# Optimization experiments

Hardware: AMD Instinct MI355X
Metric: run time of the kernel (lower is better)

The kernel has to match this reference:

```python
import jax, jax.numpy as jnp
import numpy as np

D = 1024
H = 16
HD = D // H
EPS = 1e-5

def _layernorm(x, g, b):
    mu = jnp.mean(x, axis=-1, keepdims=True)
    var = jnp.mean(jnp.square(x - mu), axis=-1, keepdims=True)
    return (x - mu) * jax.lax.rsqrt(var + EPS) * g + b

def setup_inputs() -> dict:
    key = jax.random.key(0)
    ks = jax.random.split(key, 12)
    B, Sq, Skv = 8, 1024, 1024
    s = 1.0 / np.sqrt(D)  # xavier-ish scale
    return {
        "Q": jax.random.normal(ks[0], (B, Sq, D), jnp.float32),
        "K": jax.random.normal(ks[1], (B, Skv, D), jnp.float32),
        "key_padding_mask": jnp.ones((B, Skv), jnp.int32),
        "Wq": jax.random.normal(ks[2], (D, D), jnp.float32) * s,
        "bq": jnp.zeros((D,), jnp.float32),
        "Wk": jax.random.normal(ks[3], (D, D), jnp.float32) * s,
        "bk": jnp.zeros((D,), jnp.float32),
        "Wv": jax.random.normal(ks[4], (D, D), jnp.float32) * s,
        "bv": jnp.zeros((D,), jnp.float32),
        "Wp": jax.random.normal(ks[5], (D, D), jnp.float32) * s,
        "bp": jnp.zeros((D,), jnp.float32),
        "g0": jnp.ones((D,), jnp.float32),
        "beta0": jnp.zeros((D,), jnp.float32),
        "g1": jnp.ones((D,), jnp.float32),
        "beta1": jnp.zeros((D,), jnp.float32),
    }

def reference(Q, K, key_padding_mask, Wq, bq, Wk, bk, Wv, bv, Wp, bp, g0, beta0, g1, beta1):
    B, Sq, _ = Q.shape
    q = Q @ Wq + bq                      # [B,Sq,D]
    k = K @ Wk + bk                      # [B,Skv,D]
    v = K @ Wv + bv
    qh = q.reshape(B, Sq, H, HD).transpose(0, 2, 1, 3)   # [B,H,Sq,hd]
    kh = k.reshape(B, -1, H, HD).transpose(0, 2, 1, 3)   # [B,H,Skv,hd]
    vh = v.reshape(B, -1, H, HD).transpose(0, 2, 1, 3)
    attn = jnp.einsum('bhqd,bhkd->bhqk', qh, kh) / np.sqrt(HD)
    pad = (key_padding_mask == 0)[:, None, None, :]      # [B,1,1,Skv]
    attn = jnp.where(pad, -jnp.inf, attn)
    attn = jax.nn.softmax(attn, axis=-1)
    ctx = jnp.einsum('bhqk,bhkd->bhqd', attn, vh)        # [B,H,Sq,hd]
    ctx = ctx.transpose(0, 2, 1, 3).reshape(B, Sq, H * HD)
    o = _layernorm(q + ctx, g0, beta0)
    o = _layernorm(o + jax.nn.gelu(o @ Wp + bp, approximate=False), g1, beta1)
    return o
```

## Files before the change

kernel.cpp:

```cpp
#include <hip/hip_runtime.h>
#include <hip/hip_bf16.h>
#include <math.h>

#define DEV __device__ __forceinline__

typedef __bf16 bf16;
typedef __bf16 bf16x8 __attribute__((ext_vector_type(8)));
typedef __bf16 bf16x4 __attribute__((ext_vector_type(4)));
typedef __bf16 bf16x2 __attribute__((ext_vector_type(2)));
typedef float f32x4 __attribute__((ext_vector_type(4)));
typedef float f32x16 __attribute__((ext_vector_type(16)));
typedef int i32x2 __attribute__((ext_vector_type(2)));
typedef unsigned int u32;
typedef unsigned long long u64;

static constexpr int BATCH = 8, S = 1024, D = 1024, H = 16, HD = 64;
static constexpr int M = BATCH * S;

static constexpr float QSCALE = 0.18033688f;

DEV f32x4 mfma16(bf16x8 a, bf16x8 b, f32x4 c) {
  return __builtin_amdgcn_mfma_f32_16x16x32_bf16(a, b, c, 0, 0, 0);
}
DEV f32x16 mfma32(bf16x8 a, bf16x8 b, f32x16 c) {
  return __builtin_amdgcn_mfma_f32_32x32x16_bf16(a, b, c, 0, 0, 0);
}

DEV void gload_lds16(const void* g, void* l) {
  __builtin_amdgcn_global_load_lds(
      (__attribute__((address_space(1))) void*)(g),
      (__attribute__((address_space(3))) void*)(l), 16, 0, 0);
}

DEV bf16x8 lds_read8(const void* base, int byteoff) {
  return *(const bf16x8*)((const char*)base + byteoff);
}

DEV u32 packbf(float a, float b) {
  bf16x2 t = { (bf16)a, (bf16)b };
  return __builtin_bit_cast(u32, t);
}


__global__ void cvt_bf16_kernel(const float* __restrict__ in0, bf16* __restrict__ out0,
                                const float* __restrict__ in1, bf16* __restrict__ out1, int n) {
  const float* in = blockIdx.y ? in1 : in0;
  bf16* out = blockIdx.y ? out1 : out0;
  int i = (blockIdx.x * blockDim.x + threadIdx.x) * 4;
  int stride = gridDim.x * blockDim.x * 4;
  for (; i < n; i += stride) {
    float4 v = *(const float4*)(in + i);
    bf16x4 o = { (bf16)v.x, (bf16)v.y, (bf16)v.z, (bf16)v.w };
    *(bf16x4*)(out + i) = o;
  }
}

__global__ void transpose_cvt_kernel(const float* __restrict__ w0, bf16* __restrict__ o0,
                                     const float* __restrict__ w1, bf16* __restrict__ o1,
                                     const float* __restrict__ w2, bf16* __restrict__ o2,
                                     const float* __restrict__ w3, bf16* __restrict__ o3) {
  const int z = blockIdx.z;
  const float* in = z == 0 ? w0 : z == 1 ? w1 : z == 2 ? w2 : w3;
  bf16* out = z == 0 ? o0 : z == 1 ? o1 : z == 2 ? o2 : o3;
  __shared__ float t[32][33];
  int n0 = blockIdx.x * 32, k0 = blockIdx.y * 32;
  int tx = threadIdx.x, ty = threadIdx.y;
  for (int i = 0; i < 32; i += 8)
    t[ty + i][tx] = in[(size_t)(k0 + ty + i) * D + n0 + tx];
  __syncthreads();
  for (int i = 0; i < 32; i += 8)
    out[(size_t)(n0 + ty + i) * D + k0 + tx] = (bf16)t[tx][ty + i];
}


template<int MODE>
DEV void gemm_body(const bf16* A, const bf16* Bt, const float* bias,
                   float* Cf, bf16* Cb, float osc,
                   bf16* As, bf16* Bs) {
  constexpr int K = 1024, N = 1024, BK = 32;
  const int tid = threadIdx.x, lane = tid & 63, wave = tid >> 6;
  int f = blockIdx.y * 8 + blockIdx.x;
  f = (f & 7) * 64 + (f >> 3);
  const int bm = f >> 3, bn = f & 7;
  const int wr = wave >> 1, wc = wave & 1;
  f32x4 acc[4][4] = {};
  const char* Ab = (const char*)(A + (size_t)bm * 128 * K);
  const char* Bb = (const char*)(Bt + (size_t)bn * 128 * K);

  for (int kt = 0; kt < K / BK; ++kt) {
    __syncthreads();
    const int k0b = kt * (BK * 2);
    for (int i = 0; i < 2; ++i) {
      int cbase = (wave * 2 + i) * 1024;
      int off = cbase + lane * 16;
      int row = off >> 6, col = off & 63;
      gload_lds16(Ab + (size_t)row * (K * 2) + k0b + col, (char*)As + cbase);
      gload_lds16(Bb + (size_t)row * (K * 2) + k0b + col, (char*)Bs + cbase);
    }
    __syncthreads();
    bf16x8 af[4], bfr[4];
    for (int mi = 0; mi < 4; ++mi)
      af[mi] = lds_read8(As, (wr * 64 + mi * 16 + (lane & 15)) * 64 + (lane >> 4) * 16);
    for (int ni = 0; ni < 4; ++ni)
      bfr[ni] = lds_read8(Bs, (wc * 64 + ni * 16 + (lane & 15)) * 64 + (lane >> 4) * 16);
    for (int mi = 0; mi < 4; ++mi)
      for (int ni = 0; ni < 4; ++ni)
        acc[mi][ni] = mfma16(af[mi], bfr[ni], acc[mi][ni]);
  }

  const int rbase = bm * 128 + wr * 64;
  const int cbase = bn * 128 + wc * 64;
  for (int ni = 0; ni < 4; ++ni) {
    int col = cbase + ni * 16 + (lane & 15);
    float bv = bias[col];
    for (int mi = 0; mi < 4; ++mi) {
      int row0 = rbase + mi * 16 + (lane >> 4) * 4;
      for (int r = 0; r < 4; ++r) {
        float v = acc[mi][ni][r] + bv;
        size_t idx = (size_t)(row0 + r) * N + col;
        if (MODE == 0) { Cf[idx] = v; Cb[idx] = (bf16)(v * osc); }
        if (MODE == 1) { Cb[idx] = (bf16)v; }
        if (MODE == 2) { Cf[idx] = v; }
      }
    }
  }
}

__global__ __launch_bounds__(256) void gemm_qkv_kernel(
    const bf16* __restrict__ Qb, const bf16* __restrict__ Kb,
    const bf16* __restrict__ Wqt, const bf16* __restrict__ Wkt, const bf16* __restrict__ Wvt,
    const float* __restrict__ bq, const float* __restrict__ bk, const float* __restrict__ bv,
    float* __restrict__ qf, bf16* __restrict__ qb,
    bf16* __restrict__ kb, bf16* __restrict__ vb)
{
  __shared__ bf16 As[128 * 32];
  __shared__ bf16 Bs[128 * 32];
  const int z = blockIdx.z;
  if (z == 0)      gemm_body<0>(Qb, Wqt, bq, qf, qb, QSCALE, As, Bs);
  else if (z == 1) gemm_body<1>(Kb, Wkt, bk, nullptr, kb, 1.f, As, Bs);
  else             gemm_body<1>(Kb, Wvt, bv, nullptr, vb, 1.f, As, Bs);
}

__global__ __launch_bounds__(256) void gemm_p_kernel(
    const bf16* __restrict__ A, const bf16* __restrict__ Bt,
    const float* __restrict__ bias, float* __restrict__ Cf)
{
  __shared__ bf16 As[128 * 32];
  __shared__ bf16 Bs[128 * 32];
  gemm_body<2>(A, Bt, bias, Cf, nullptr, 1.f, As, Bs);
}


DEV int swz(int row, int colb) { return row * 128 + (colb ^ ((row & 7) << 4)); }

__global__ __launch_bounds__(256, 3) void attn_kernel(
    const bf16* __restrict__ q, const bf16* __restrict__ k, const bf16* __restrict__ v,
    const int* __restrict__ mask, float* __restrict__ ctx)
{
  __shared__ bf16 Kl[2][64 * 64];
  __shared__ bf16 Vt[2][64 * 64];
  const int tid = threadIdx.x, lane = tid & 63, wave = tid >> 6;
  const int hi = lane >> 5, lq = lane & 31;
  const int wg = blockIdx.x;
  const int xcd = wg & 7, ix = wg >> 3;
  const int bh = xcd * 16 + (ix & 15);
  const int qt = ix >> 4;
  const int b = bh >> 4, h = bh & 15;
  const int q0 = qt * 128 + wave * 32;
  const size_t base = (size_t)b * S * D + (size_t)h * HD;

  bf16x8 qf[4];
#pragma unroll
  for (int hc = 0; hc < 4; ++hc)
    qf[hc] = *(const bf16x8*)(q + base + (size_t)(q0 + lq) * D + hc * 16 + hi * 8);

  f32x16 oaccT[2] = {};
  float mrow = -3e38f, lrow = 0.f;

  bf16x8 kst[2], vst[2];
  const int koff = tid * 16;
  const int krow = koff >> 7, kcol = koff & 127;

#define LOADK(KV0)                                                              \
  {                                                                             \
    _Pragma("unroll")                                                           \
    for (int rr = 0; rr < 2; ++rr)                                              \
      kst[rr] = *(const bf16x8*)((const char*)(k + base +                       \
                 (size_t)((KV0) + rr * 32 + krow) * D) + kcol);                 \
    _Pragma("unroll")                                                           \
    for (int rr = 0; rr < 2; ++rr) {                                            \
      int kvr = rr * 32 + wave * 8;                                             \
      _Pragma("unroll")                                                         \
      for (int i = 0; i < 8; ++i)                                               \
        vst[rr][i] = v[base + (size_t)((KV0) + kvr + i) * D + lane];            \
    }                                                                           \
  }

#define WRITEK(BI)                                                              \
  {                                                                             \
    _Pragma("unroll")                                                           \
    for (int rr = 0; rr < 2; ++rr)                                              \
      *(bf16x8*)((char*)Kl[BI] + swz(rr * 32 + krow, kcol)) = kst[rr];          \
    _Pragma("unroll")                                                           \
    for (int rr = 0; rr < 2; ++rr)                                              \
      *(bf16x8*)((char*)Vt[BI] + swz(lane, (rr * 32 + wave * 8) * 2)) = vst[rr];\
  }

  LOADK(0);
  WRITEK(0);

  for (int kt = 0; kt < S / 64; ++kt) {
    const int cur = kt & 1;
    const int kv0 = kt * 64;
    __syncthreads();
    if (kt < S / 64 - 1) LOADK(kv0 + 64);

    const char* Kb_ = (const char*)Kl[cur];
    const char* Vb_ = (const char*)Vt[cur];

    u64 mv = __ballot(mask[b * S + kv0 + lane] != 0);

    f32x16 sacc[2];
    __builtin_amdgcn_s_setprio(1);
#pragma unroll
    for (int sub = 0; sub < 2; ++sub) {
      f32x16 a = {};
#pragma unroll
      for (int hc = 0; hc < 4; ++hc) {
        bf16x8 kf = lds_read8(Kb_, swz(sub * 32 + lq, hc * 32 + hi * 16));
        a = mfma32(kf, qf[hc], a);
      }
      sacc[sub] = a;
    }
    __builtin_amdgcn_s_setprio(0);

    float mx = -3e38f;
    if (mv == ~0ull) {
#pragma unroll
      for (int sub = 0; sub < 2; ++sub)
#pragma unroll
        for (int r = 0; r < 16; ++r) mx = fmaxf(mx, sacc[sub][r]);
    } else {
      u64 mqh = mv >> (hi * 4);
#pragma unroll
      for (int sub = 0; sub < 2; ++sub)
#pragma unroll
        for (int rr = 0; rr < 4; ++rr)
#pragma unroll
          for (int rm = 0; rm < 4; ++rm) {
            int reg = rr * 4 + rm;
            bool ok = (mqh >> (rm + 8 * rr + 32 * sub)) & 1ull;
            float s = ok ? sacc[sub][reg] : -1e30f;
            sacc[sub][reg] = s;
            mx = fmaxf(mx, s);
          }
    }
    mx = fmaxf(mx, __shfl_xor(mx, 32));

    if (__any(mx > mrow + 11.5f)) {
      float mnew = fmaxf(mrow, mx);
      float fsc = exp2f(mrow - mnew);
      mrow = mnew;
      lrow *= fsc;
      oaccT[0] *= fsc;
      oaccT[1] *= fsc;
    }

    float rs = 0.f;
    u32 W[2][4][2];
#pragma unroll
    for (int sub = 0; sub < 2; ++sub)
#pragma unroll
      for (int rr = 0; rr < 4; ++rr)
#pragma unroll
        for (int hh = 0; hh < 2; ++hh) {
          float p0 = exp2f(sacc[sub][rr * 4 + 2 * hh] - mrow);
          float p1 = exp2f(sacc[sub][rr * 4 + 2 * hh + 1] - mrow);
          rs += p0 + p1;
          W[sub][rr][hh] = packbf(p0, p1);
        }
    rs += __shfl_xor(rs, 32);
    lrow += rs;

    bf16x8 pfr[4];
#pragma unroll
    for (int t = 0; t < 4; ++t) {
      const int sub = t >> 1, r0 = 2 * (t & 1);
      i32x2 s0 = __builtin_amdgcn_permlane32_swap(
          (int)W[sub][r0][0], (int)W[sub][r0 + 1][0], false, false);
      i32x2 s1 = __builtin_amdgcn_permlane32_swap(
          (int)W[sub][r0][1], (int)W[sub][r0 + 1][1], false, false);
      u32 wd[4] = { (u32)s0[0], (u32)s1[0], (u32)s0[1], (u32)s1[1] };
      pfr[t] = __builtin_bit_cast(bf16x8, wd);
    }

    __builtin_amdgcn_s_setprio(1);
#pragma unroll
    for (int hdsub = 0; hdsub < 2; ++hdsub) {
      f32x16 a = oaccT[hdsub];
#pragma unroll
      for (int t = 0; t < 4; ++t) {
        bf16x8 vf = lds_read8(Vb_, swz(hdsub * 32 + lq, t * 32 + hi * 16));
        a = mfma32(vf, pfr[t], a);
      }
      oaccT[hdsub] = a;
    }
    __builtin_amdgcn_s_setprio(0);

    if (kt < S / 64 - 1) WRITEK(cur ^ 1);
  }

  float linv = 1.0f / lrow;
  size_t rowb = ((size_t)b * S + q0 + lq) * D + (size_t)h * HD;
#pragma unroll
  for (int hdsub = 0; hdsub < 2; ++hdsub)
#pragma unroll
    for (int rr = 0; rr < 4; ++rr) {
      f32x4 o = { oaccT[hdsub][rr * 4 + 0] * linv, oaccT[hdsub][rr * 4 + 1] * linv,
                  oaccT[hdsub][rr * 4 + 2] * linv, oaccT[hdsub][rr * 4 + 3] * linv };
      *(f32x4*)(ctx + rowb + 32 * hdsub + 8 * rr + 4 * hi) = o;
    }
}


DEV void block_stats(float s, float s2, float* red, int tid, float& mu, float& rstd) {
  for (int off = 32; off > 0; off >>= 1) {
    s += __shfl_down(s, off);
    s2 += __shfl_down(s2, off);
  }
  int wave = tid >> 6, lane = tid & 63;
  if (lane == 0) { red[wave] = s; red[4 + wave] = s2; }
  __syncthreads();
  float S1 = red[0] + red[1] + red[2] + red[3];
  float S2 = red[4] + red[5] + red[6] + red[7];
  mu = S1 * (1.f / 1024.f);
  rstd = rsqrtf(S2 * (1.f / 1024.f) - mu * mu + 1e-5f);
}

__global__ __launch_bounds__(256) void ln0_kernel(
    const float* __restrict__ qf, const float* __restrict__ ctx,
    const float* __restrict__ g, const float* __restrict__ beta,
    float* __restrict__ of, bf16* __restrict__ ob)
{
  __shared__ float red[8];
  const int row = blockIdx.x, tid = threadIdx.x;
  const size_t base = (size_t)row * D;
  float4 x = *(const float4*)(qf + base + tid * 4);
  float4 c = *(const float4*)(ctx + base + tid * 4);
  x.x += c.x; x.y += c.y; x.z += c.z; x.w += c.w;
  float mu, rstd;
  block_stats(x.x + x.y + x.z + x.w,
              x.x * x.x + x.y * x.y + x.z * x.z + x.w * x.w, red, tid, mu, rstd);
  float4 gv = *(const float4*)(g + tid * 4);
  float4 bv = *(const float4*)(beta + tid * 4);
  float o0 = (x.x - mu) * rstd * gv.x + bv.x;
  float o1 = (x.y - mu) * rstd * gv.y + bv.y;
  float o2 = (x.z - mu) * rstd * gv.z + bv.z;
  float o3 = (x.w - mu) * rstd * gv.w + bv.w;
  *(float4*)(of + base + tid * 4) = make_float4(o0, o1, o2, o3);
  bf16x4 o = { (bf16)o0, (bf16)o1, (bf16)o2, (bf16)o3 };
  *(bf16x4*)(ob + base + tid * 4) = o;
}

DEV float gelu_exact(float t) { return 0.5f * t * (1.f + erff(t * 0.70710678118654752f)); }

__global__ __launch_bounds__(256) void ln1_kernel(
    const float* __restrict__ of, const float* __restrict__ pf,
    const float* __restrict__ g, const float* __restrict__ beta,
    float* __restrict__ out)
{
  __shared__ float red[8];
  const int row = blockIdx.x, tid = threadIdx.x;
  const size_t base = (size_t)row * D;
  float4 x = *(const float4*)(of + base + tid * 4);
  float4 p = *(const float4*)(pf + base + tid * 4);
  x.x += gelu_exact(p.x); x.y += gelu_exact(p.y);
  x.z += gelu_exact(p.z); x.w += gelu_exact(p.w);
  float mu, rstd;
  block_stats(x.x + x.y + x.z + x.w,
              x.x * x.x + x.y * x.y + x.z * x.z + x.w * x.w, red, tid, mu, rstd);
  float4 gv = *(const float4*)(g + tid * 4);
  float4 bv = *(const float4*)(beta + tid * 4);
  float o0 = (x.x - mu) * rstd * gv.x + bv.x;
  float o1 = (x.y - mu) * rstd * gv.y + bv.y;
  float o2 = (x.z - mu) * rstd * gv.z + bv.z;
  float o3 = (x.w - mu) * rstd * gv.w + bv.w;
  *(float4*)(out + base + tid * 4) = make_float4(o0, o1, o2, o3);
}


extern "C" void kernel_launch(void* const* d_in, const int* in_sizes, int n_in,
                              void* d_out, int out_size, void* d_ws, size_t ws_size,
                              hipStream_t stream) {
  const float* Q     = (const float*)d_in[0];
  const float* K     = (const float*)d_in[1];
  const int*   mask  = (const int*)d_in[2];
  const float* Wq    = (const float*)d_in[3];
  const float* bq    = (const float*)d_in[4];
  const float* Wk    = (const float*)d_in[5];
  const float* bk    = (const float*)d_in[6];
  const float* Wv    = (const float*)d_in[7];
  const float* bv    = (const float*)d_in[8];
  const float* Wp    = (const float*)d_in[9];
  const float* bp    = (const float*)d_in[10];
  const float* g0    = (const float*)d_in[11];
  const float* beta0 = (const float*)d_in[12];
  const float* g1    = (const float*)d_in[13];
  const float* beta1 = (const float*)d_in[14];
  float* out = (float*)d_out;

  char* w = (char*)d_ws;
  const size_t MB = 1u << 20;
  bf16* Qb  = (bf16*)(w + 0 * MB);
  bf16* Kb  = (bf16*)(w + 16 * MB);
  bf16* Wqt = (bf16*)(w + 32 * MB);
  bf16* Wkt = (bf16*)(w + 34 * MB);
  bf16* Wvt = (bf16*)(w + 36 * MB);
  bf16* Wpt = (bf16*)(w + 38 * MB);
  float* qf = (float*)(w + 40 * MB);
  bf16* qb  = (bf16*)(w + 72 * MB);
  bf16* kb  = (bf16*)(w + 88 * MB);
  bf16* vb  = (bf16*)(w + 104 * MB);
  float* ctx = (float*)(w + 120 * MB);
  float* pf  = ctx;
  float* of  = (float*)(w + 152 * MB);
  bf16* ob   = (bf16*)(w + 0 * MB);

  dim3 cg(1024, 2);
  cvt_bf16_kernel<<<cg, 256, 0, stream>>>(Q, Qb, K, Kb, M * D);
  dim3 tb(32, 8), tg(32, 32, 4);
  transpose_cvt_kernel<<<tg, tb, 0, stream>>>(Wq, Wqt, Wk, Wkt, Wv, Wvt, Wp, Wpt);

  dim3 gq(8, 64, 3);
  gemm_qkv_kernel<<<gq, 256, 0, stream>>>(Qb, Kb, Wqt, Wkt, Wvt, bq, bk, bv, qf, qb, kb, vb);

  attn_kernel<<<1024, 256, 0, stream>>>(qb, kb, vb, mask, ctx);

  ln0_kernel<<<M, 256, 0, stream>>>(qf, ctx, g0, beta0, of, ob);
  dim3 gp(8, 64);
  gemm_p_kernel<<<gp, 256, 0, stream>>>(ob, Wpt, bp, pf);
  ln1_kernel<<<M, 256, 0, stream>>>(of, pf, g1, beta1, out);
}
```

Measured before the change: 363.2 us.

## Store GEMM intermediates in bf16 only and XOR-swizzle GEMM LDS tiles

Drops the fp32 copies of the Q projection, the LayerNorm-0 output and the Wp projection, so the downstream LayerNorm kernels read bf16 (and rescale the pre-scaled q back up) instead of fp32. This cuts global write and read traffic across several kernels. The GEMM's LDS loads and reads now use an XOR swizzle on 16-byte column slots to reduce bank conflicts. In exchange, the residual paths for both LayerNorms and the GELU input are rounded to bf16, which adds error.

```diff
diff --git a/kernel.cpp b/kernel.cpp
--- a/kernel.cpp
+++ b/kernel.cpp
@@ -18,6 +18,7 @@
 static constexpr int M = BATCH * S;
 
 static constexpr float QSCALE = 0.18033688f;
+static constexpr float INVQSCALE = 5.54517744f;
 
 DEV f32x4 mfma16(bf16x8 a, bf16x8 b, f32x4 c) {
   return __builtin_amdgcn_mfma_f32_16x16x32_bf16(a, b, c, 0, 0, 0);
@@ -73,12 +74,11 @@
 }
 
 
-template<int MODE>
 DEV void gemm_body(const bf16* A, const bf16* Bt, const float* bias,
-                   float* Cf, bf16* Cb, float osc,
-                   bf16* As, bf16* Bs) {
+                   bf16* Cb, float osc, bf16* As, bf16* Bs) {
   constexpr int K = 1024, N = 1024, BK = 32;
   const int tid = threadIdx.x, lane = tid & 63, wave = tid >> 6;
+  const int lo = lane & 15, g = lane >> 4;
   int f = blockIdx.y * 8 + blockIdx.x;
   f = (f & 7) * 64 + (f >> 3);
   const int bm = f >> 3, bn = f & 7;
@@ -87,22 +87,29 @@
   const char* Ab = (const char*)(A + (size_t)bm * 128 * K);
   const char* Bb = (const char*)(Bt + (size_t)bn * 128 * K);
 
+  const int srow[2] = { (wave * 2 + 0) * 16 + (lane >> 2), (wave * 2 + 1) * 16 + (lane >> 2) };
+  const int sslot = lane & 3;
+
   for (int kt = 0; kt < K / BK; ++kt) {
     __syncthreads();
     const int k0b = kt * (BK * 2);
     for (int i = 0; i < 2; ++i) {
       int cbase = (wave * 2 + i) * 1024;
-      int off = cbase + lane * 16;
-      int row = off >> 6, col = off & 63;
-      gload_lds16(Ab + (size_t)row * (K * 2) + k0b + col, (char*)As + cbase);
-      gload_lds16(Bb + (size_t)row * (K * 2) + k0b + col, (char*)Bs + cbase);
+      int row = srow[i];
+      int scol = ((sslot ^ (row & 3)) << 4);
+      gload_lds16(Ab + (size_t)row * (K * 2) + k0b + scol, (char*)As + cbase);
+      gload_lds16(Bb + (size_t)row * (K * 2) + k0b + scol, (char*)Bs + cbase);
     }
     __syncthreads();
     bf16x8 af[4], bfr[4];
-    for (int mi = 0; mi < 4; ++mi)
-      af[mi] = lds_read8(As, (wr * 64 + mi * 16 + (lane & 15)) * 64 + (lane >> 4) * 16);
-    for (int ni = 0; ni < 4; ++ni)
-      bfr[ni] = lds_read8(Bs, (wc * 64 + ni * 16 + (lane & 15)) * 64 + (lane >> 4) * 16);
+    for (int mi = 0; mi < 4; ++mi) {
+      int ar = wr * 64 + mi * 16 + lo;
+      af[mi] = lds_read8(As, ar * 64 + ((g ^ (ar & 3)) << 4));
+    }
+    for (int ni = 0; ni < 4; ++ni) {
+      int br = wc * 64 + ni * 16 + lo;
+      bfr[ni] = lds_read8(Bs, br * 64 + ((g ^ (br & 3)) << 4));
+    }
     for (int mi = 0; mi < 4; ++mi)
       for (int ni = 0; ni < 4; ++ni)
         acc[mi][ni] = mfma16(af[mi], bfr[ni], acc[mi][ni]);
@@ -111,16 +118,13 @@
   const int rbase = bm * 128 + wr * 64;
   const int cbase = bn * 128 + wc * 64;
   for (int ni = 0; ni < 4; ++ni) {
-    int col = cbase + ni * 16 + (lane & 15);
+    int col = cbase + ni * 16 + lo;
     float bv = bias[col];
     for (int mi = 0; mi < 4; ++mi) {
-      int row0 = rbase + mi * 16 + (lane >> 4) * 4;
+      int row0 = rbase + mi * 16 + g * 4;
       for (int r = 0; r < 4; ++r) {
         float v = acc[mi][ni][r] + bv;
-        size_t idx = (size_t)(row0 + r) * N + col;
-        if (MODE == 0) { Cf[idx] = v; Cb[idx] = (bf16)(v * osc); }
-        if (MODE == 1) { Cb[idx] = (bf16)v; }
-        if (MODE == 2) { Cf[idx] = v; }
+        Cb[(size_t)(row0 + r) * N + col] = (bf16)(v * osc);
       }
     }
   }
@@ -130,24 +134,23 @@
     const bf16* __restrict__ Qb, const bf16* __restrict__ Kb,
     const bf16* __restrict__ Wqt, const bf16* __restrict__ Wkt, const bf16* __restrict__ Wvt,
     const float* __restrict__ bq, const float* __restrict__ bk, const float* __restrict__ bv,
-    float* __restrict__ qf, bf16* __restrict__ qb,
-    bf16* __restrict__ kb, bf16* __restrict__ vb)
+    bf16* __restrict__ qb, bf16* __restrict__ kb, bf16* __restrict__ vb)
 {
   __shared__ bf16 As[128 * 32];
   __shared__ bf16 Bs[128 * 32];
   const int z = blockIdx.z;
-  if (z == 0)      gemm_body<0>(Qb, Wqt, bq, qf, qb, QSCALE, As, Bs);
-  else if (z == 1) gemm_body<1>(Kb, Wkt, bk, nullptr, kb, 1.f, As, Bs);
-  else             gemm_body<1>(Kb, Wvt, bv, nullptr, vb, 1.f, As, Bs);
+  if (z == 0)      gemm_body(Qb, Wqt, bq, qb, QSCALE, As, Bs);
+  else if (z == 1) gemm_body(Kb, Wkt, bk, kb, 1.f, As, Bs);
+  else             gemm_body(Kb, Wvt, bv, vb, 1.f, As, Bs);
 }
 
 __global__ __launch_bounds__(256) void gemm_p_kernel(
     const bf16* __restrict__ A, const bf16* __restrict__ Bt,
-    const float* __restrict__ bias, float* __restrict__ Cf)
+    const float* __restrict__ bias, bf16* __restrict__ Cb)
 {
   __shared__ bf16 As[128 * 32];
   __shared__ bf16 Bs[128 * 32];
-  gemm_body<2>(A, Bt, bias, Cf, nullptr, 1.f, As, Bs);
+  gemm_body(A, Bt, bias, Cb, 1.f, As, Bs);
 }
 
 
@@ -338,53 +341,56 @@
 }
 
 __global__ __launch_bounds__(256) void ln0_kernel(
-    const float* __restrict__ qf, const float* __restrict__ ctx,
+    const bf16* __restrict__ qb, const float* __restrict__ ctx,
     const float* __restrict__ g, const float* __restrict__ beta,
-    float* __restrict__ of, bf16* __restrict__ ob)
+    bf16* __restrict__ ob)
 {
   __shared__ float red[8];
   const int row = blockIdx.x, tid = threadIdx.x;
   const size_t base = (size_t)row * D;
-  float4 x = *(const float4*)(qf + base + tid * 4);
+  bf16x4 qv = *(const bf16x4*)(qb + base + tid * 4);
   float4 c = *(const float4*)(ctx + base + tid * 4);
-  x.x += c.x; x.y += c.y; x.z += c.z; x.w += c.w;
+  float x0 = (float)qv[0] * INVQSCALE + c.x;
+  float x1 = (float)qv[1] * INVQSCALE + c.y;
+  float x2 = (float)qv[2] * INVQSCALE + c.z;
+  float x3 = (float)qv[3] * INVQSCALE + c.w;
   float mu, rstd;
-  block_stats(x.x + x.y + x.z + x.w,
-              x.x * x.x + x.y * x.y + x.z * x.z + x.w * x.w, red, tid, mu, rstd);
+  block_stats(x0 + x1 + x2 + x3,
+              x0 * x0 + x1 * x1 + x2 * x2 + x3 * x3, red, tid, mu, rstd);
   float4 gv = *(const float4*)(g + tid * 4);
   float4 bv = *(const float4*)(beta + tid * 4);
-  float o0 = (x.x - mu) * rstd * gv.x + bv.x;
-  float o1 = (x.y - mu) * rstd * gv.y + bv.y;
-  float o2 = (x.z - mu) * rstd * gv.z + bv.z;
-  float o3 = (x.w - mu) * rstd * gv.w + bv.w;
-  *(float4*)(of + base + tid * 4) = make_float4(o0, o1, o2, o3);
-  bf16x4 o = { (bf16)o0, (bf16)o1, (bf16)o2, (bf16)o3 };
+  bf16x4 o = { (bf16)((x0 - mu) * rstd * gv.x + bv.x),
+               (bf16)((x1 - mu) * rstd * gv.y + bv.y),
+               (bf16)((x2 - mu) * rstd * gv.z + bv.z),
+               (bf16)((x3 - mu) * rstd * gv.w + bv.w) };
   *(bf16x4*)(ob + base + tid * 4) = o;
 }
 
 DEV float gelu_exact(float t) { return 0.5f * t * (1.f + erff(t * 0.70710678118654752f)); }
 
 __global__ __launch_bounds__(256) void ln1_kernel(
-    const float* __restrict__ of, const float* __restrict__ pf,
+    const bf16* __restrict__ ob, const bf16* __restrict__ pb,
     const float* __restrict__ g, const float* __restrict__ beta,
     float* __restrict__ out)
 {
   __shared__ float red[8];
   const int row = blockIdx.x, tid = threadIdx.x;
   const size_t base = (size_t)row * D;
-  float4 x = *(const float4*)(of + base + tid * 4);
-  float4 p = *(const float4*)(pf + base + tid * 4);
-  x.x += gelu_exact(p.x); x.y += gelu_exact(p.y);
-  x.z += gelu_exact(p.z); x.w += gelu_exact(p.w);
+  bf16x4 ov = *(const bf16x4*)(ob + base + tid * 4);
+  bf16x4 pv = *(const bf16x4*)(pb + base + tid * 4);
+  float x0 = (float)ov[0] + gelu_exact((float)pv[0]);
+  float x1 = (float)ov[1] + gelu_exact((float)pv[1]);
+  float x2 = (float)ov[2] + gelu_exact((float)pv[2]);
+  float x3 = (float)ov[3] + gelu_exact((float)pv[3]);
   float mu, rstd;
-  block_stats(x.x + x.y + x.z + x.w,
-              x.x * x.x + x.y * x.y + x.z * x.z + x.w * x.w, red, tid, mu, rstd);
+  block_stats(x0 + x1 + x2 + x3,
+              x0 * x0 + x1 * x1 + x2 * x2 + x3 * x3, red, tid, mu, rstd);
   float4 gv = *(const float4*)(g + tid * 4);
   float4 bv = *(const float4*)(beta + tid * 4);
-  float o0 = (x.x - mu) * rstd * gv.x + bv.x;
-  float o1 = (x.y - mu) * rstd * gv.y + bv.y;
-  float o2 = (x.z - mu) * rstd * gv.z + bv.z;
-  float o3 = (x.w - mu) * rstd * gv.w + bv.w;
+  float o0 = (x0 - mu) * rstd * gv.x + bv.x;
+  float o1 = (x1 - mu) * rstd * gv.y + bv.y;
+  float o2 = (x2 - mu) * rstd * gv.z + bv.z;
+  float o3 = (x3 - mu) * rstd * gv.w + bv.w;
   *(float4*)(out + base + tid * 4) = make_float4(o0, o1, o2, o3);
 }
 
@@ -417,14 +423,12 @@
   bf16* Wkt = (bf16*)(w + 34 * MB);
   bf16* Wvt = (bf16*)(w + 36 * MB);
   bf16* Wpt = (bf16*)(w + 38 * MB);
-  float* qf = (float*)(w + 40 * MB);
-  bf16* qb  = (bf16*)(w + 72 * MB);
-  bf16* kb  = (bf16*)(w + 88 * MB);
-  bf16* vb  = (bf16*)(w + 104 * MB);
-  float* ctx = (float*)(w + 120 * MB);
-  float* pf  = ctx;
-  float* of  = (float*)(w + 152 * MB);
-  bf16* ob   = (bf16*)(w + 0 * MB);
+  bf16* qb  = (bf16*)(w + 40 * MB);
+  bf16* kb  = (bf16*)(w + 56 * MB);
+  bf16* vb  = (bf16*)(w + 72 * MB);
+  float* ctx = (float*)(w + 88 * MB);
+  bf16* pb  = (bf16*)(w + 120 * MB);
+  bf16* ob  = (bf16*)(w + 0 * MB);
 
   dim3 cg(1024, 2);
   cvt_bf16_kernel<<<cg, 256, 0, stream>>>(Q, Qb, K, Kb, M * D);
@@ -432,12 +436,12 @@
   transpose_cvt_kernel<<<tg, tb, 0, stream>>>(Wq, Wqt, Wk, Wkt, Wv, Wvt, Wp, Wpt);
 
   dim3 gq(8, 64, 3);
-  gemm_qkv_kernel<<<gq, 256, 0, stream>>>(Qb, Kb, Wqt, Wkt, Wvt, bq, bk, bv, qf, qb, kb, vb);
+  gemm_qkv_kernel<<<gq, 256, 0, stream>>>(Qb, Kb, Wqt, Wkt, Wvt, bq, bk, bv, qb, kb, vb);
 
   attn_kernel<<<1024, 256, 0, stream>>>(qb, kb, vb, mask, ctx);
 
-  ln0_kernel<<<M, 256, 0, stream>>>(qf, ctx, g0, beta0, of, ob);
+  ln0_kernel<<<M, 256, 0, stream>>>(qb, ctx, g0, beta0, ob);
   dim3 gp(8, 64);
-  gemm_p_kernel<<<gp, 256, 0, stream>>>(ob, Wpt, bp, pf);
-  ln1_kernel<<<M, 256, 0, stream>>>(of, pf, g1, beta1, out);
-}
+  gemm_p_kernel<<<gp, 256, 0, stream>>>(ob, Wpt, bp, pb);
+  ln1_kernel<<<M, 256, 0, stream>>>(ob, pb, g1, beta1, out);
+}
```

Result: faster. 340.7 us (-6.2%).
